# Performance work log

Hardware: AMD Instinct MI355X
Metric: run time of the kernel (lower is better)

## Reference

```python
import math
import jax, jax.numpy as jnp
import numpy as np

D_MODEL = 1024
N_HEADS = 16
HEAD_DIM = D_MODEL // N_HEADS
D_FF = 4096
LN_EPS = 1e-5


def _layer_norm(x, g, b):
    mu = jnp.mean(x, axis=-1, keepdims=True)
    var = jnp.var(x, axis=-1, keepdims=True)
    return (x - mu) * jax.lax.rsqrt(var + LN_EPS) * g + b


def setup_inputs() -> dict:
    key = jax.random.key(0)
    ks = jax.random.split(key, 8)
    s = 0.02
    d, dff = D_MODEL, D_FF
    return {
        "src": jax.random.normal(ks[0], (2, 2048, d), dtype=jnp.float32),
        "in_proj_w": jax.random.normal(ks[1], (3 * d, d), dtype=jnp.float32) * s,
        "in_proj_b": jnp.zeros((3 * d,), dtype=jnp.float32),
        "out_w": jax.random.normal(ks[2], (d, d), dtype=jnp.float32) * s,
        "out_b": jnp.zeros((d,), dtype=jnp.float32),
        "lin1_w": jax.random.normal(ks[3], (dff, d), dtype=jnp.float32) * s,
        "lin1_b": jnp.zeros((dff,), dtype=jnp.float32),
        "lin2_w": jax.random.normal(ks[4], (d, dff), dtype=jnp.float32) * s,
        "lin2_b": jnp.zeros((d,), dtype=jnp.float32),
        "ln1_g": jnp.ones((d,), dtype=jnp.float32),
        "ln1_b": jnp.zeros((d,), dtype=jnp.float32),
        "ln2_g": jnp.ones((d,), dtype=jnp.float32),
        "ln2_b": jnp.zeros((d,), dtype=jnp.float32),
    }


def reference(src, in_proj_w, in_proj_b, out_w, out_b, lin1_w, lin1_b,
              lin2_w, lin2_b, ln1_g, ln1_b, ln2_g, ln2_b):
    B, S, d = src.shape
    # QKV projections (in_proj_weight split at d, then kv split)
    q = src @ in_proj_w[:d].T + in_proj_b[:d]              # [B,S,d]
    kv = src @ in_proj_w[d:].T + in_proj_b[d:]             # [B,S,2d]
    q = q.reshape(B, S, N_HEADS, HEAD_DIM)
    kv = kv.reshape(B, S, 2, N_HEADS, HEAD_DIM)
    k, v = kv[:, :, 0], kv[:, :, 1]
    softmax_scale = 1.0 / math.sqrt(HEAD_DIM)
    scores = jnp.einsum('bthd,bshd->bhts', q, k) * softmax_scale  # [B,H,Sq,Skv]
    # 'distribute': softmax over the QUERY dimension (dim=-2)
    attention = jax.nn.softmax(scores, axis=-2)
    post = jnp.einsum('bhts,bshd->bthd', attention, v)     # [B,Sq,H,hd]
    # post-attention activation 'gelu' (torch exact gelu)
    post = jax.nn.gelu(post, approximate=False)
    # attention_scale == 'sqrt': divide by sqrt(kv_len)
    post = post / math.sqrt(S)
    attn_out = post.reshape(B, S, d) @ out_w.T + out_b
    # post-norm residual structure (pre_norm=False, dropout=0)
    x = _layer_norm(src + attn_out, ln1_g, ln1_b)
    ff = jax.nn.gelu(x @ lin1_w.T + lin1_b, approximate=False) @ lin2_w.T + lin2_b
    return _layer_norm(x + ff, ln2_g, ln2_b)
```

## Files before the change

kernel.cpp:

```cpp
#include <hip/hip_runtime.h>
#include <hip/hip_bf16.h>
#include <math.h>


using bf16x8 = __attribute__((ext_vector_type(8))) short;
using f32x4  = __attribute__((ext_vector_type(4))) float;

__device__ inline f32x4 mfma16(bf16x8 a, bf16x8 b, f32x4 c) {
    return __builtin_amdgcn_mfma_f32_16x16x32_bf16(a, b, c, 0, 0, 0);
}

__device__ inline ushort f2bf(float f) {
    union { float f; unsigned u; } x; x.f = f;
    unsigned r = x.u + 0x7fffu + ((x.u >> 16) & 1u);
    return (ushort)(r >> 16);
}

__device__ inline float bf2f(ushort u) {
    union { unsigned u; float f; } x; x.u = ((unsigned)u) << 16; return x.f;
}

__device__ inline unsigned pk2bf(float a, float b) {
    __hip_bfloat162 h = __float22bfloat162_rn(float2{a, b});
    union { __hip_bfloat162 h; unsigned u; } x; x.h = h;
    return x.u;
}

__device__ inline float gelu_fast(float v) {
    float u = v * (1.5957691216f + 0.0713548162f * v * v);
    float e = __expf(u);
    return v * (e / (e + 1.0f));
}

__device__ __forceinline__ void gl2lds16(const ushort* g, ushort* l) {
    __builtin_amdgcn_global_load_lds(
        (const __attribute__((address_space(1))) unsigned int*)g,
        (__attribute__((address_space(3))) unsigned int*)l,
        16, 0, 0);
}

__global__ __launch_bounds__(256) void cvt_all(const float4* __restrict__ s0,
                                               const float4* __restrict__ s1,
                                               const float4* __restrict__ s2,
                                               const float4* __restrict__ s3,
                                               const float4* __restrict__ s4,
                                               ushort4* __restrict__ out) {
    int i = blockIdx.x * 256 + threadIdx.x;
    const float4* p;
    int off;
    if (i < 1048576)      { p = s0; off = i; }
    else if (i < 1835008) { p = s1; off = i - 1048576; }
    else if (i < 2097152) { p = s2; off = i - 1835008; }
    else if (i < 3145728) { p = s3; off = i - 2097152; }
    else                  { p = s4; off = i - 3145728; }
    float4 v = p[off];
    ushort4 o;
    o.x = f2bf(v.x); o.y = f2bf(v.y); o.z = f2bf(v.z); o.w = f2bf(v.w);
    out[i] = o;
}

__global__ __launch_bounds__(256) void gemm_bt(
    const ushort* __restrict__ A, const ushort* __restrict__ Bw,
    const float* __restrict__ bias, int M, int N, int K, int kLen, int mode, int gx,
    ushort* __restrict__ ob0, ushort* __restrict__ ob1, ushort* __restrict__ ob2) {
    __shared__ ushort As[2][128 * 32];
    __shared__ ushort Bs[2][128 * 32];
    int tid = threadIdx.x, lane = tid & 63, w = tid >> 6;
    int wm = w >> 1, wn = w & 1;

    int Nx = gridDim.x, Ny = gridDim.y;
    int bx = blockIdx.x, by = blockIdx.y;
    int gy = 8 / gx;
    if ((Nx % gx) == 0 && (Ny % gy) == 0 && ((Nx * Ny) & 7) == 0) {
        int Sx = Nx / gx, Sy = Ny / gy;
        int i = bx + Nx * by;
        int c = i & 7, j = i >> 3;
        int cx = c % gx, cy = c / gx;
        bx = cx * Sx + j % Sx;
        by = cy * Sy + (j / Sx) % Sy;
    }
    int bm = by * 128, bn = bx * 128;
    int kz = blockIdx.z;
    int q4 = lane >> 4, l15 = lane & 15;
    f32x4 acc[4][4] = {};

    int srow = w * 16 + (lane >> 2);
    int scg = lane & 3;
    const ushort* Ab = A + (size_t)bm * K + (size_t)kz * kLen;
    const ushort* Bb = Bw + (size_t)bn * K + (size_t)kz * kLen;
    const ushort* gA0 = Ab + (size_t)srow * K + scg * 8;
    const ushort* gA1 = Ab + (size_t)(64 + srow) * K + scg * 8;
    const ushort* gB0 = Bb + (size_t)srow * K + scg * 8;
    const ushort* gB1 = Bb + (size_t)(64 + srow) * K + scg * 8;
    ushort* lA00 = As[0] + w * 512;
    ushort* lA10 = As[0] + 2048 + w * 512;
    ushort* lB00 = Bs[0] + w * 512;
    ushort* lB10 = Bs[0] + 2048 + w * 512;
    ushort* lA01 = As[1] + w * 512;
    ushort* lA11 = As[1] + 2048 + w * 512;
    ushort* lB01 = Bs[1] + w * 512;
    ushort* lB11 = Bs[1] + 2048 + w * 512;

    const ushort* aB[2] = { &As[0][(wm * 64 + l15) * 32 + q4 * 8],
                            &As[1][(wm * 64 + l15) * 32 + q4 * 8] };
    const ushort* bB[2] = { &Bs[0][(wn * 64 + l15) * 32 + q4 * 8],
                            &Bs[1][(wn * 64 + l15) * 32 + q4 * 8] };

    for (int k0 = 0; k0 < kLen; k0 += 64) {
        __syncthreads();
        gl2lds16(gA0 + k0, lA00);
        gl2lds16(gA1 + k0, lA10);
        gl2lds16(gB0 + k0, lB00);
        gl2lds16(gB1 + k0, lB10);
        gl2lds16(gA0 + k0 + 32, lA01);
        gl2lds16(gA1 + k0 + 32, lA11);
        gl2lds16(gB0 + k0 + 32, lB01);
        gl2lds16(gB1 + k0 + 32, lB11);
        __syncthreads();
#pragma unroll
        for (int u = 0; u < 2; u++) {
            bf16x8 af[4], bfr[4];
#pragma unroll
            for (int mi = 0; mi < 4; mi++)
                af[mi] = *(const bf16x8*)(aB[u] + mi * 512);
#pragma unroll
            for (int ni = 0; ni < 4; ni++)
                bfr[ni] = *(const bf16x8*)(bB[u] + ni * 512);
#pragma unroll
            for (int mi = 0; mi < 4; mi++)
#pragma unroll
                for (int ni = 0; ni < 4; ni++)
                    acc[mi][ni] = mfma16(af[mi], bfr[ni], acc[mi][ni]);
        }
    }

    int r0 = bm + wm * 64, c0 = bn + wn * 64;
#pragma unroll
    for (int mi = 0; mi < 4; mi++) {
#pragma unroll
        for (int ni = 0; ni < 4; ni++) {
            int colg = c0 + ni * 16 + l15;
            float bv = (mode == 3) ? 0.f : bias[colg];
#pragma unroll
            for (int r = 0; r < 4; r++) {
                int rowg = r0 + mi * 16 + q4 * 4 + r;
                float v = acc[mi][ni][r] + bv;
                if (mode == 0) {
                    if (colg < 1024) {
                        ob0[(size_t)rowg * 1024 + colg] = f2bf(v);
                    } else if (colg < 2048) {
                        ob1[(size_t)rowg * 1024 + (colg - 1024)] = f2bf(v);
                    } else {
                        ob2[(size_t)rowg * 1024 + (colg - 2048)] = f2bf(v);
                    }
                } else if (mode == 2) {
                    ob0[(size_t)rowg * N + colg] = f2bf(gelu_fast(v));
                } else {
                    ob0[(size_t)kz * M * N + (size_t)rowg * N + colg] = f2bf(v);
                }
            }
        }
    }
}

__global__ __launch_bounds__(256) void attn_colsum_part(const ushort* __restrict__ qb,
                                                        const ushort* __restrict__ kb,
                                                        float* __restrict__ csum) {
    __shared__ ushort Qs[64 * 64];
    int tid = threadIdx.x, lane = tid & 63, w = tid >> 6;
    int id = blockIdx.x;
    int th = id & 1, sblk = (id >> 1) & 15, bh = id >> 5;
    int b = bh >> 4, h = bh & 15;
    int q4 = lane >> 4, l15 = lane & 15;
    const ushort* qbase = qb + (size_t)(b * 2048) * 1024 + h * 64;
    const ushort* kbase = kb + (size_t)(b * 2048) * 1024 + h * 64;
    int s_base = sblk * 128 + w * 32;

    bf16x8 ka[2][2];
#pragma unroll
    for (int mi = 0; mi < 2; mi++) {
        const ushort* kp = kbase + (size_t)(s_base + mi * 16 + l15) * 1024 + q4 * 8;
        ka[mi][0] = *(const bf16x8*)(kp);
        ka[mi][1] = *(const bf16x8*)(kp + 32);
    }
    float acc[2][4] = {};

    int rl = lane >> 3;
    int cswz = (((lane & 7) ^ rl) << 3);
    int swf = l15 & 7;
    int c0s = (q4 ^ swf) << 3;
    int c1s = ((q4 + 4) ^ swf) << 3;
    int tEnd = th * 1024 + 1024;
    for (int t0 = th * 1024; t0 < tEnd; t0 += 64) {
        __syncthreads();
        gl2lds16(qbase + (size_t)(t0 + w * 16 + rl) * 1024 + cswz, Qs + (w * 16) * 64);
        gl2lds16(qbase + (size_t)(t0 + w * 16 + 8 + rl) * 1024 + cswz, Qs + (w * 16 + 8) * 64);
        __syncthreads();
#pragma unroll
        for (int tsub = 0; tsub < 4; tsub++) {
            int rQ = (tsub * 16 + l15) * 64;
            bf16x8 bq0 = *(const bf16x8*)&Qs[rQ + c0s];
            bf16x8 bq1 = *(const bf16x8*)&Qs[rQ + c1s];
#pragma unroll
            for (int mi = 0; mi < 2; mi++) {
                f32x4 d = {0.f, 0.f, 0.f, 0.f};
                d = mfma16(ka[mi][0], bq0, d);
                d = mfma16(ka[mi][1], bq1, d);
#pragma unroll
                for (int r = 0; r < 4; r++)
                    acc[mi][r] += __expf(d[r] * 0.125f);
            }
        }
    }
#pragma unroll
    for (int mi = 0; mi < 2; mi++)
#pragma unroll
        for (int r = 0; r < 4; r++) {
            float v = acc[mi][r];
            v += __shfl_xor(v, 1); v += __shfl_xor(v, 2);
            v += __shfl_xor(v, 4); v += __shfl_xor(v, 8);
            if (l15 == 0)
                csum[(size_t)th * 65536 + (size_t)bh * 2048 + s_base + mi * 16 + q4 * 4 + r] = v;
        }
}

__global__ __launch_bounds__(256) void foldv(const ushort* __restrict__ vrow,
                                             const float* __restrict__ csum,
                                             ushort* __restrict__ vt) {
    __shared__ ushort T[64 * 72];
    int tid = threadIdx.x;
    int bh = blockIdx.x >> 5, sch = blockIdx.x & 31;
    int b = bh >> 4, h = bh & 15;
    int s0 = sch * 64;
    int sl = tid >> 3, dh8 = (tid & 7) * 8;
#pragma unroll
    for (int rep = 0; rep < 2; rep++) {
        int s = sl + rep * 32;
        size_t ci = (size_t)bh * 2048 + s0 + s;
        float n = 1.f / (csum[ci] + csum[65536 + ci]);
        const ushort* p = vrow + (size_t)(b * 2048 + s0 + s) * 1024 + h * 64 + dh8;
        ushort4 u0 = ((const ushort4*)p)[0];
        ushort4 u1 = ((const ushort4*)p)[1];
        ushort4 o0, o1;
        o0.x = f2bf(bf2f(u0.x) * n); o0.y = f2bf(bf2f(u0.y) * n);
        o0.z = f2bf(bf2f(u0.z) * n); o0.w = f2bf(bf2f(u0.w) * n);
        o1.x = f2bf(bf2f(u1.x) * n); o1.y = f2bf(bf2f(u1.y) * n);
        o1.z = f2bf(bf2f(u1.z) * n); o1.w = f2bf(bf2f(u1.w) * n);
        *(ushort4*)&T[s * 72 + dh8] = o0;
        *(ushort4*)&T[s * 72 + dh8 + 4] = o1;
    }
    __syncthreads();
    int dhl = tid >> 3, soff = (tid & 7) * 8;
#pragma unroll
    for (int rep = 0; rep < 2; rep++) {
        int d = dhl + rep * 32;
        ushort tmp[8];
#pragma unroll
        for (int j = 0; j < 8; j++) tmp[j] = T[(soff + j) * 72 + d];
        *(uint4*)(vt + ((size_t)bh * 64 + d) * 2048 + s0 + soff) = *(uint4*)tmp;
    }
}

__global__ __launch_bounds__(256) void attn_pv_split(const ushort* __restrict__ qb,
                                                     const ushort* __restrict__ kb,
                                                     const ushort* __restrict__ vt,
                                                     ushort* __restrict__ opart) {
    __shared__ ushort Ks[64 * 64];
    __shared__ ushort Vs[64 * 64];
    __shared__ ushort Ps[4][32 * 68];
    int tid = threadIdx.x, lane = tid & 63, w = tid >> 6;
    int id = blockIdx.x;
    int sh = id & 1, tblk = (id >> 1) & 15, bh = id >> 5;
    int b = bh >> 4, h = bh & 15;
    int q4 = lane >> 4, l15 = lane & 15;
    const ushort* qbase = qb + (size_t)(b * 2048) * 1024 + h * 64;
    const ushort* kbase = kb + (size_t)(b * 2048) * 1024 + h * 64;
    const ushort* vtb = vt + (size_t)bh * 64 * 2048;
    int t_base = tblk * 128 + w * 32;

    bf16x8 aq[2][2];
#pragma unroll
    for (int mi = 0; mi < 2; mi++) {
        const ushort* qp = qbase + (size_t)(t_base + mi * 16 + l15) * 1024 + q4 * 8;
        aq[mi][0] = *(const bf16x8*)(qp);
        aq[mi][1] = *(const bf16x8*)(qp + 32);
    }
    f32x4 oacc[2][4] = {};
    ushort* myP = Ps[w];

    int rl = lane >> 3;
    int cswz = (((lane & 7) ^ rl) << 3);
    int swf = l15 & 7;
    int c0s = (q4 ^ swf) << 3;
    int c1s = ((q4 + 4) ^ swf) << 3;
    int sEnd = sh * 1024 + 1024;
    for (int s0 = sh * 1024; s0 < sEnd; s0 += 64) {
        __syncthreads();
        gl2lds16(kbase + (size_t)(s0 + w * 16 + rl) * 1024 + cswz, Ks + (w * 16) * 64);
        gl2lds16(kbase + (size_t)(s0 + w * 16 + 8 + rl) * 1024 + cswz, Ks + (w * 16 + 8) * 64);
        gl2lds16(vtb + (size_t)(w * 16 + rl) * 2048 + s0 + cswz, Vs + (w * 16) * 64);
        gl2lds16(vtb + (size_t)(w * 16 + 8 + rl) * 2048 + s0 + cswz, Vs + (w * 16 + 8) * 64);
        __syncthreads();
#pragma unroll
        for (int ssub = 0; ssub < 4; ssub++) {
            int rA = (ssub * 16 + l15) * 64;
            bf16x8 bk0 = *(const bf16x8*)&Ks[rA + c0s];
            bf16x8 bk1 = *(const bf16x8*)&Ks[rA + c1s];
#pragma unroll
            for (int mi = 0; mi < 2; mi++) {
                f32x4 d = {0.f, 0.f, 0.f, 0.f};
                d = mfma16(bk0, aq[mi][0], d);
                d = mfma16(bk1, aq[mi][1], d);
                float p0 = __expf(d[0] * 0.125f);
                float p1 = __expf(d[1] * 0.125f);
                float p2 = __expf(d[2] * 0.125f);
                float p3 = __expf(d[3] * 0.125f);
                uint2 uu;
                uu.x = pk2bf(p0, p1);
                uu.y = pk2bf(p2, p3);
                *(uint2*)&myP[(mi * 16 + l15) * 68 + ssub * 16 + q4 * 4] = uu;
            }
        }
#pragma unroll
        for (int mi = 0; mi < 2; mi++) {
            bf16x8 ap0 = *(const bf16x8*)&myP[(mi * 16 + l15) * 68 + q4 * 8];
            bf16x8 ap1 = *(const bf16x8*)&myP[(mi * 16 + l15) * 68 + 32 + q4 * 8];
#pragma unroll
            for (int ni = 0; ni < 4; ni++) {
                int rV = (ni * 16 + l15) * 64;
                bf16x8 bv0 = *(const bf16x8*)&Vs[rV + c0s];
                bf16x8 bv1 = *(const bf16x8*)&Vs[rV + c1s];
                oacc[mi][ni] = mfma16(ap0, bv0, oacc[mi][ni]);
                oacc[mi][ni] = mfma16(ap1, bv1, oacc[mi][ni]);
            }
        }
    }
    ushort* op = opart + (size_t)sh * 4096 * 1024;
#pragma unroll
    for (int mi = 0; mi < 2; mi++)
#pragma unroll
        for (int ni = 0; ni < 4; ni++)
#pragma unroll
            for (int r = 0; r < 4; r++) {
                int t = t_base + mi * 16 + q4 * 4 + r;
                op[(size_t)(b * 2048 + t) * 1024 + h * 64 + ni * 16 + l15] =
                    f2bf(oacc[mi][ni][r]);
            }
}

__global__ __launch_bounds__(256) void attn_combine(const ushort* __restrict__ opart,
                                                    ushort* __restrict__ post) {
    const size_t PLANE = (size_t)4096 * 1024;
    size_t base = ((size_t)blockIdx.x * 256 + threadIdx.x) * 8;
    ushort4 a0 = *(const ushort4*)(opart + base);
    ushort4 a1 = *(const ushort4*)(opart + base + 4);
    ushort4 b0 = *(const ushort4*)(opart + PLANE + base);
    ushort4 b1 = *(const ushort4*)(opart + PLANE + base + 4);
    const float sc = 0.022097086912079608f;
    ushort4 o0, o1;
    o0.x = f2bf(gelu_fast(bf2f(a0.x) + bf2f(b0.x)) * sc);
    o0.y = f2bf(gelu_fast(bf2f(a0.y) + bf2f(b0.y)) * sc);
    o0.z = f2bf(gelu_fast(bf2f(a0.z) + bf2f(b0.z)) * sc);
    o0.w = f2bf(gelu_fast(bf2f(a0.w) + bf2f(b0.w)) * sc);
    o1.x = f2bf(gelu_fast(bf2f(a1.x) + bf2f(b1.x)) * sc);
    o1.y = f2bf(gelu_fast(bf2f(a1.y) + bf2f(b1.y)) * sc);
    o1.z = f2bf(gelu_fast(bf2f(a1.z) + bf2f(b1.z)) * sc);
    o1.w = f2bf(gelu_fast(bf2f(a1.w) + bf2f(b1.w)) * sc);
    *(ushort4*)(post + base) = o0;
    *(ushort4*)(post + base + 4) = o1;
}

__global__ __launch_bounds__(256) void ln_comb4(const ushort* __restrict__ parts,
                                                const float* __restrict__ bias,
                                                const float* __restrict__ res,
                                                const float* __restrict__ gw,
                                                const float* __restrict__ bw,
                                                ushort* __restrict__ outb,
                                                float* __restrict__ outf) {
    const size_t PLANE = (size_t)4096 * 1024;
    int row = blockIdx.x, tid = threadIdx.x;
    int lane = tid & 63, wid = tid >> 6;
    size_t off = (size_t)row * 1024 + tid * 4;
    float4 r = *(const float4*)(res + off);
    float4 bb = *(const float4*)(bias + tid * 4);
    float4 v;
    v.x = r.x + bb.x; v.y = r.y + bb.y; v.z = r.z + bb.z; v.w = r.w + bb.w;
#pragma unroll
    for (int p = 0; p < 4; p++) {
        ushort4 u = *(const ushort4*)(parts + p * PLANE + off);
        v.x += bf2f(u.x); v.y += bf2f(u.y); v.z += bf2f(u.z); v.w += bf2f(u.w);
    }
    float s = v.x + v.y + v.z + v.w;
    float ss = v.x * v.x + v.y * v.y + v.z * v.z + v.w * v.w;
    for (int m = 1; m < 64; m <<= 1) { s += __shfl_xor(s, m); ss += __shfl_xor(ss, m); }
    __shared__ float red[8];
    if (lane == 0) { red[wid] = s; red[wid + 4] = ss; }
    __syncthreads();
    s = red[0] + red[1] + red[2] + red[3];
    ss = red[4] + red[5] + red[6] + red[7];
    float mu = s * (1.f / 1024.f);
    float var = ss * (1.f / 1024.f) - mu * mu;
    float inv = rsqrtf(var + 1e-5f);
    float4 gv = *(const float4*)(gw + tid * 4);
    float4 bv = *(const float4*)(bw + tid * 4);
    float o0 = (v.x - mu) * inv * gv.x + bv.x;
    float o1 = (v.y - mu) * inv * gv.y + bv.y;
    float o2 = (v.z - mu) * inv * gv.z + bv.z;
    float o3 = (v.w - mu) * inv * gv.w + bv.w;
    if (outf) {
        float4 o; o.x = o0; o.y = o1; o.z = o2; o.w = o3;
        *(float4*)(outf + off) = o;
    }
    if (outb) {
        ushort4 o; o.x = f2bf(o0); o.y = f2bf(o1); o.z = f2bf(o2); o.w = f2bf(o3);
        *(ushort4*)(outb + off) = o;
    }
}

extern "C" void kernel_launch(void* const* d_in, const int* in_sizes, int n_in,
                              void* d_out, int out_size, void* d_ws, size_t ws_size,
                              hipStream_t stream) {
    const float* src  = (const float*)d_in[0];
    const float* w_in = (const float*)d_in[1];
    const float* b_in = (const float*)d_in[2];
    const float* w_o  = (const float*)d_in[3];
    const float* b_o  = (const float*)d_in[4];
    const float* w1   = (const float*)d_in[5];
    const float* b1   = (const float*)d_in[6];
    const float* w2   = (const float*)d_in[7];
    const float* b2   = (const float*)d_in[8];
    const float* g1   = (const float*)d_in[9];
    const float* be1  = (const float*)d_in[10];
    const float* g2   = (const float*)d_in[11];
    const float* be2  = (const float*)d_in[12];
    float* out = (float*)d_out;

    const size_t M = 4096;
    char* wsp = (char*)d_ws;
    size_t off = 0;
    auto alloc = [&](size_t bytes) -> void* {
        void* p = wsp + off;
        off = (off + bytes + 255) & ~(size_t)255;
        return p;
    };
    ushort* src_bf  = (ushort*)alloc(M * 1024 * 2);
    ushort* win_bf  = (ushort*)alloc(3072 * 1024 * 2);
    ushort* wout_bf = (ushort*)alloc(1024 * 1024 * 2);
    ushort* w1_bf   = (ushort*)alloc(4096 * 1024 * 2);
    ushort* w2_bf   = (ushort*)alloc((size_t)1024 * 4096 * 2);
    ushort* q_bf    = (ushort*)alloc(M * 1024 * 2);
    ushort* k_bf    = (ushort*)alloc(M * 1024 * 2);
    ushort* vt_bf   = (ushort*)alloc(M * 1024 * 2);
    ushort* post_bf = (ushort*)alloc(M * 1024 * 2);
    ushort* part    = (ushort*)alloc(4 * M * 1024 * 2);
    float*  csum    = (float*)alloc(2 * 32 * 2048 * 4);
    ushort* x_bf    = (ushort*)alloc(M * 1024 * 2);
    float*  x_f32   = (float*)alloc(M * 1024 * 4);
    ushort* h1_bf   = (ushort*)alloc(M * 4096 * 2);
    ushort* v_row   = part;
    ushort* opart   = part + M * 1024;

    cvt_all<<<16384, 256, 0, stream>>>((const float4*)src, (const float4*)w_in,
                                       (const float4*)w_o, (const float4*)w1,
                                       (const float4*)w2, (ushort4*)src_bf);

    gemm_bt<<<dim3(24, 32, 1), 256, 0, stream>>>(src_bf, win_bf, b_in, 4096, 3072, 1024, 1024, 0, 2,
                                                 q_bf, k_bf, v_row);

    attn_colsum_part<<<1024, 256, 0, stream>>>(q_bf, k_bf, csum);
    foldv<<<1024, 256, 0, stream>>>(v_row, csum, vt_bf);
    attn_pv_split<<<1024, 256, 0, stream>>>(q_bf, k_bf, vt_bf, opart);
    attn_combine<<<2048, 256, 0, stream>>>(opart, post_bf);

    gemm_bt<<<dim3(8, 32, 4), 256, 0, stream>>>(post_bf, wout_bf, b_o, 4096, 1024, 1024, 256, 3, 1,
                                                part, nullptr, nullptr);
    ln_comb4<<<4096, 256, 0, stream>>>(part, b_o, src, g1, be1, x_bf, x_f32);

    gemm_bt<<<dim3(32, 32, 1), 256, 0, stream>>>(x_bf, w1_bf, b1, 4096, 4096, 1024, 1024, 2, 2,
                                                 h1_bf, nullptr, nullptr);
    gemm_bt<<<dim3(8, 32, 4), 256, 0, stream>>>(h1_bf, w2_bf, b2, 4096, 1024, 4096, 1024, 3, 1,
                                                part, nullptr, nullptr);
    ln_comb4<<<4096, 256, 0, stream>>>(part, b2, x_f32, g2, be2, nullptr, out);
}
```

Before: 465.8 us.

## Transpose GEMM MFMA output for vectorized stores; remap attention blocks per XCD

The GEMM swaps the MFMA operand order so each lane holds four consecutive output columns of one row. This lets the epilogue load the bias as a float4 and write packed 8-byte bf16 stores instead of scattered 2-byte stores. The attention colsum, foldv and PV kernels remap block IDs so every block of a given batch-head lands on the same XCD, which should improve L2 reuse of that head's Q/K/V data. The remap assumes round-robin dispatch of blocks across 8 XCDs and a grid size divisible accordingly.

```diff
diff --git a/kernel.cpp b/kernel.cpp
--- a/kernel.cpp
+++ b/kernel.cpp
@@ -130,34 +130,42 @@
             for (int mi = 0; mi < 4; mi++)
 #pragma unroll
                 for (int ni = 0; ni < 4; ni++)
-                    acc[mi][ni] = mfma16(af[mi], bfr[ni], acc[mi][ni]);
+                    acc[mi][ni] = mfma16(bfr[ni], af[mi], acc[mi][ni]);
         }
     }
 
     int r0 = bm + wm * 64, c0 = bn + wn * 64;
 #pragma unroll
     for (int mi = 0; mi < 4; mi++) {
+        int rowg = r0 + mi * 16 + l15;
 #pragma unroll
         for (int ni = 0; ni < 4; ni++) {
-            int colg = c0 + ni * 16 + l15;
-            float bv = (mode == 3) ? 0.f : bias[colg];
-#pragma unroll
-            for (int r = 0; r < 4; r++) {
-                int rowg = r0 + mi * 16 + q4 * 4 + r;
-                float v = acc[mi][ni][r] + bv;
-                if (mode == 0) {
-                    if (colg < 1024) {
-                        ob0[(size_t)rowg * 1024 + colg] = f2bf(v);
-                    } else if (colg < 2048) {
-                        ob1[(size_t)rowg * 1024 + (colg - 1024)] = f2bf(v);
-                    } else {
-                        ob2[(size_t)rowg * 1024 + (colg - 2048)] = f2bf(v);
-                    }
-                } else if (mode == 2) {
-                    ob0[(size_t)rowg * N + colg] = f2bf(gelu_fast(v));
+            int colb = c0 + ni * 16 + q4 * 4;
+            float v0 = acc[mi][ni][0], v1 = acc[mi][ni][1];
+            float v2 = acc[mi][ni][2], v3 = acc[mi][ni][3];
+            if (mode != 3) {
+                float4 bb = *(const float4*)(bias + colb);
+                v0 += bb.x; v1 += bb.y; v2 += bb.z; v3 += bb.w;
+            }
+            if (mode == 2) {
+                v0 = gelu_fast(v0); v1 = gelu_fast(v1);
+                v2 = gelu_fast(v2); v3 = gelu_fast(v3);
+            }
+            uint2 uu;
+            uu.x = pk2bf(v0, v1);
+            uu.y = pk2bf(v2, v3);
+            if (mode == 0) {
+                if (colb < 1024) {
+                    *(uint2*)&ob0[(size_t)rowg * 1024 + colb] = uu;
+                } else if (colb < 2048) {
+                    *(uint2*)&ob1[(size_t)rowg * 1024 + (colb - 1024)] = uu;
                 } else {
-                    ob0[(size_t)kz * M * N + (size_t)rowg * N + colg] = f2bf(v);
+                    *(uint2*)&ob2[(size_t)rowg * 1024 + (colb - 2048)] = uu;
                 }
+            } else if (mode == 2) {
+                *(uint2*)&ob0[(size_t)rowg * N + colb] = uu;
+            } else {
+                *(uint2*)&ob0[(size_t)kz * M * N + (size_t)rowg * N + colb] = uu;
             }
         }
     }
@@ -169,7 +177,9 @@
     __shared__ ushort Qs[64 * 64];
     int tid = threadIdx.x, lane = tid & 63, w = tid >> 6;
     int id = blockIdx.x;
-    int th = id & 1, sblk = (id >> 1) & 15, bh = id >> 5;
+    int xcd = id & 7, g = id >> 3;
+    int sub = g & 31, bh = (g >> 5) * 8 + xcd;
+    int th = sub & 1, sblk = sub >> 1;
     int b = bh >> 4, h = bh & 15;
     int q4 = lane >> 4, l15 = lane & 15;
     const ushort* qbase = qb + (size_t)(b * 2048) * 1024 + h * 64;
@@ -229,7 +239,9 @@
                                              ushort* __restrict__ vt) {
     __shared__ ushort T[64 * 72];
     int tid = threadIdx.x;
-    int bh = blockIdx.x >> 5, sch = blockIdx.x & 31;
+    int id = blockIdx.x;
+    int xcd = id & 7, g = id >> 3;
+    int sch = g & 31, bh = (g >> 5) * 8 + xcd;
     int b = bh >> 4, h = bh & 15;
     int s0 = sch * 64;
     int sl = tid >> 3, dh8 = (tid & 7) * 8;
@@ -270,7 +282,9 @@
     __shared__ ushort Ps[4][32 * 68];
     int tid = threadIdx.x, lane = tid & 63, w = tid >> 6;
     int id = blockIdx.x;
-    int sh = id & 1, tblk = (id >> 1) & 15, bh = id >> 5;
+    int xcd = id & 7, g = id >> 3;
+    int sub = g & 31, bh = (g >> 5) * 8 + xcd;
+    int sh = sub & 1, tblk = sub >> 1;
     int b = bh >> 4, h = bh & 15;
     int q4 = lane >> 4, l15 = lane & 15;
     const ushort* qbase = qb + (size_t)(b * 2048) * 1024 + h * 64;
```

After: 441.7 us. -5.2%, faster.
